# Kernel optimization log

Measured on AMD Instinct MI355X. Metric: run time of the kernel, lower is better.

Reference implementation:

```python
import jax, jax.numpy as jnp
import numpy as np
import math

B, S, D, H, E = 4, 4096, 256, 8, 262144
HD = D // H
ITER_NUM = 4
TEMP = 1.0
LN_EPS = 1e-12
N = B * S


def setup_inputs() -> dict:
    key = jax.random.key(0)
    ks = jax.random.split(key, 6)
    return {
        "hidden_states": jax.random.normal(ks[0], (B, S, D), dtype=jnp.float32),
        "attention_mask": jnp.zeros((B, S), dtype=jnp.float32),
        "src": jax.random.randint(ks[1], (E,), 0, N),
        "dst": jax.random.randint(ks[2], (E,), 0, N),
        "Wqkv": jax.random.normal(ks[3], (D, 3 * D), dtype=jnp.float32) * 0.02,
        "bqkv": jnp.zeros((3 * D,), dtype=jnp.float32),
        "Wo": jax.random.normal(ks[4], (D, D), dtype=jnp.float32) * 0.02,
        "bo": jnp.zeros((D,), dtype=jnp.float32),
        "gamma": jnp.ones((D,), dtype=jnp.float32),
        "beta": jnp.zeros((D,), dtype=jnp.float32),
    }


def _gn_attn(hidden_states, attention_mask, src, dst, Wqkv, bqkv, Wo, bo, gamma, beta):
    # qkv projection (node ordering is batch-major: node = b*S + s)
    qkv = hidden_states @ Wqkv + bqkv                      # [B,S,3D]
    q, k, v = jnp.split(qkv, 3, axis=-1)
    q = q / math.sqrt(HD)
    qn = q.reshape(N, H, HD)
    kn = k.reshape(N, H, HD)
    vn = v.reshape(N, H, HD)
    node_mask = (attention_mask >= 0).reshape(N)           # [N] bool

    # per-edge dot-product scores: u_dot_v('k','q') -> dot(k[src], q[dst])
    score = jnp.einsum("ehd,ehd->eh", kn[src], qn[dst])    # [E,H]
    edge_mask = node_mask[src] & node_mask[dst]
    score = jnp.where(edge_mask[:, None], score, jnp.float32(-10000.0))

    # edge softmax over incoming edges of each dst node (per head)
    mx = jax.ops.segment_max(score, dst, num_segments=N)   # [N,H]
    es = jnp.exp(score - mx[dst])
    den = jax.ops.segment_sum(es, dst, num_segments=N)     # [N,H]
    attn = es / den[dst]                                   # [E,H]

    # diffusion (heat-kernel / PPR-style) message passing
    h = math.exp(-TEMP) * vn                               # [N,H,HD]
    gather = h
    fact = 1.0
    for ki in range(1, ITER_NUM):
        msg = attn[:, :, None] * h[src]                    # [E,H,HD]
        h = jax.ops.segment_sum(msg, dst, num_segments=N)  # [N,H,HD]
        fact = fact * (TEMP / ki)
        gather = gather + fact * h

    attn_out = gather.reshape(B, S, D)

    # output projection + residual + LayerNorm
    y = attn_out @ Wo + bo + hidden_states
    mu = jnp.mean(y, axis=-1, keepdims=True)
    var = jnp.mean(jnp.square(y - mu), axis=-1, keepdims=True)
    return (y - mu) / jnp.sqrt(var + LN_EPS) * gamma + beta


def reference(hidden_states, attention_mask, src, dst, Wqkv, bqkv, Wo, bo, gamma, beta):
    return _gn_attn(hidden_states, attention_mask, src, dst, Wqkv, bqkv, Wo, bo, gamma, beta)
```

## Files before the change

kernel.cpp:

```cpp
#include <hip/hip_runtime.h>
#include <math.h>

#define NN 16384
#define DD 256
#define HH 8
#define EE 262144
#define D3 768
#define QSCALE 0.17677669529663687f
#define EXPN1 0.36787944117144233f
#define LN_EPS 1e-12f

typedef short bf16x8 __attribute__((ext_vector_type(8)));
typedef float f32x4 __attribute__((ext_vector_type(4)));
typedef float f32x2 __attribute__((ext_vector_type(2)));
typedef unsigned short u16;
typedef unsigned char u8;

__device__ __forceinline__ float bf_lo(unsigned u) { return __uint_as_float(u << 16); }
__device__ __forceinline__ float bf_hi(unsigned u) { return __uint_as_float(u & 0xffff0000u); }
__device__ __forceinline__ unsigned f2bf(float f) {
    unsigned b = __float_as_uint(f);
    return (b + 0x7fffu + ((b >> 16) & 1u)) >> 16;
}
__device__ __forceinline__ unsigned pack2bf(float lo, float hi) {
    return f2bf(lo) | (f2bf(hi) << 16);
}
__device__ __forceinline__ u8 f2fp8(float v) {
    return (u8)(__builtin_amdgcn_cvt_pk_fp8_f32(v, v, 0, false) & 0xff);
}

__global__ void prep_kernel(const float* __restrict__ hidden, unsigned* __restrict__ hidb,
                            const float* __restrict__ Wqkv, const float* __restrict__ bqkv,
                            u16* __restrict__ WtQ, float* __restrict__ biasq,
                            const float* __restrict__ Wo, const float* __restrict__ bo,
                            u16* __restrict__ WtO, float* __restrict__ biaso,
                            const int* __restrict__ dst, int* __restrict__ deg) {
    int b = blockIdx.x;
    if (b < 4096) {
        int gid = b * 256 + threadIdx.x;
        float4 v = *(const float4*)(hidden + (size_t)gid * 4);
        *(uint2*)(hidb + (size_t)gid * 2) = make_uint2(pack2bf(v.x, v.y), pack2bf(v.z, v.w));
    } else if (b < 4864) {
        int gid = (b - 4096) * 256 + threadIdx.x;
        int n = gid >> 8, k = gid & 255;
        float s = (n < DD) ? QSCALE : 1.0f;
        WtQ[(size_t)n * 256 + k] = (u16)f2bf(Wqkv[(size_t)k * D3 + n] * s);
        if (k == 0) biasq[n] = bqkv[n] * s;
    } else if (b < 5120) {
        int gid = (b - 4864) * 256 + threadIdx.x;
        int n = gid >> 8, k = gid & 255;
        WtO[(size_t)n * 256 + k] = (u16)f2bf(Wo[(size_t)k * DD + n]);
        if (k == 0) biaso[n] = bo[n];
    } else {
        int e = (b - 5120) * 256 + threadIdx.x;
        atomicAdd(&deg[dst[e]], 1);
    }
}

__global__ __launch_bounds__(256) void mfma_gemm1_kernel(
        const u16* __restrict__ Ab, const u16* __restrict__ Bt,
        const float* __restrict__ bias,
        u16* __restrict__ qb, u8* __restrict__ kb8,
        u8* __restrict__ h8, u16* __restrict__ gb) {
    __shared__ u16 As[128 * 40];
    __shared__ u16 Bs[128 * 40];
    const int tid = threadIdx.x;
    const int m0 = blockIdx.y * 128;
    const int n0 = blockIdx.x * 128;
    const int wave = tid >> 6, lane = tid & 63;
    const int wr = wave >> 1, wc = wave & 1;
    const int lm = lane & 15, quad = lane >> 4;

    f32x4 acc[4][4] = {};
    const int r0 = tid >> 2;
    const int c8 = (tid & 3) * 8;

    for (int k0 = 0; k0 < 256; k0 += 32) {
        #pragma unroll
        for (int s = 0; s < 2; ++s) {
            int r = r0 + s * 64;
            *(uint4*)&As[r * 40 + c8] = *(const uint4*)(Ab + (size_t)(m0 + r) * 256 + k0 + c8);
            *(uint4*)&Bs[r * 40 + c8] = *(const uint4*)(Bt + (size_t)(n0 + r) * 256 + k0 + c8);
        }
        __syncthreads();
        bf16x8 af[4], bfv[4];
        #pragma unroll
        for (int mi = 0; mi < 4; ++mi)
            af[mi] = *(const bf16x8*)&As[(wr * 64 + mi * 16 + lm) * 40 + quad * 8];
        #pragma unroll
        for (int ni = 0; ni < 4; ++ni)
            bfv[ni] = *(const bf16x8*)&Bs[(wc * 64 + ni * 16 + lm) * 40 + quad * 8];
        #pragma unroll
        for (int mi = 0; mi < 4; ++mi)
            #pragma unroll
            for (int ni = 0; ni < 4; ++ni)
                acc[mi][ni] = __builtin_amdgcn_mfma_f32_16x16x32_bf16(
                    af[mi], bfv[ni], acc[mi][ni], 0, 0, 0);
        __syncthreads();
    }

    const int type = n0 >> 8;
    const int cb = n0 & 255;
    #pragma unroll
    for (int mi = 0; mi < 4; ++mi) {
        #pragma unroll
        for (int j = 0; j < 4; ++j) {
            int m = m0 + wr * 64 + mi * 16 + quad * 4 + j;
            #pragma unroll
            for (int ni = 0; ni < 4; ++ni) {
                int nl = wc * 64 + ni * 16 + lm;
                float val = acc[mi][ni][j] + bias[n0 + nl];
                size_t off = (size_t)m * 256 + cb + nl;
                if (type == 0) qb[off] = (u16)f2bf(val);
                else if (type == 1) kb8[off] = f2fp8(val);
                else {
                    float hx = val * EXPN1;
                    h8[off] = f2fp8(hx);
                    gb[off] = (u16)f2bf(hx);
                }
            }
        }
    }
}

__global__ __launch_bounds__(1024) void scan_kernel(const int* __restrict__ deg,
                                                    int* __restrict__ offs,
                                                    int* __restrict__ cursor, int n) {
    __shared__ int part[1024];
    int t = threadIdx.x;
    int base = t * 16;
    int local[16];
    int s = 0;
    #pragma unroll
    for (int i = 0; i < 16; ++i) { local[i] = s; s += deg[base + i]; }
    part[t] = s;
    __syncthreads();
    for (int d = 1; d < 1024; d <<= 1) {
        int add = (t >= d) ? part[t - d] : 0;
        __syncthreads();
        part[t] += add;
        __syncthreads();
    }
    int excl = part[t] - s;
    #pragma unroll
    for (int i = 0; i < 16; ++i) {
        offs[base + i] = excl + local[i];
        cursor[base + i] = excl + local[i];
    }
    if (t == 1023) offs[n] = excl + s;
}

__global__ void scatter_kernel(const int* __restrict__ src, const int* __restrict__ dst,
                               int* __restrict__ cursor, int* __restrict__ srcs) {
    int e = blockIdx.x * 256 + threadIdx.x;
    int pos = atomicAdd(&cursor[dst[e]], 1);
    srcs[pos] = src[e];
}

__global__ __launch_bounds__(256) void edge_softmax_kernel(
        const unsigned* __restrict__ qb, const u8* __restrict__ kb8,
        const int* __restrict__ offs, const int* __restrict__ srcs,
        const float* __restrict__ amask, float* __restrict__ attn,
        float* __restrict__ inv) {
    const int wave = threadIdx.x >> 6, lane = threadIdx.x & 63;
    const int node = blockIdx.x * 4 + wave;
    const int h = lane & 7;
    const int eo = lane >> 3;
    const int beg = offs[node], end = offs[node + 1];
    const uint4* qp = (const uint4*)(qb + (size_t)node * 128 + h * 16);
    uint4 q0 = qp[0], q1 = qp[1], q2 = qp[2], q3 = qp[3];
    unsigned qq[16] = {q0.x, q0.y, q0.z, q0.w, q1.x, q1.y, q1.z, q1.w,
                       q2.x, q2.y, q2.z, q2.w, q3.x, q3.y, q3.z, q3.w};
    const bool dvalid = amask[node] >= 0.0f;

    float m = -1e30f;
    for (int i0 = beg; i0 < end; i0 += 8) {
        int i = i0 + eo;
        if (i < end) {
            int s = srcs[i];
            const uint4* kp = (const uint4*)(kb8 + (size_t)s * 256 + h * 32);
            uint4 k0 = kp[0], k1 = kp[1];
            unsigned kk[8] = {k0.x, k0.y, k0.z, k0.w, k1.x, k1.y, k1.z, k1.w};
            float acc = 0.0f;
            #pragma unroll
            for (int t = 0; t < 8; ++t) {
                f32x2 a = __builtin_amdgcn_cvt_pk_f32_fp8(kk[t], false);
                f32x2 b = __builtin_amdgcn_cvt_pk_f32_fp8(kk[t], true);
                acc += a.x * bf_lo(qq[2 * t]) + a.y * bf_hi(qq[2 * t]);
                acc += b.x * bf_lo(qq[2 * t + 1]) + b.y * bf_hi(qq[2 * t + 1]);
            }
            bool valid = dvalid && (amask[s] >= 0.0f);
            float score = valid ? acc : -10000.0f;
            attn[(size_t)i * 8 + h] = score;
            m = fmaxf(m, score);
        }
    }
    m = fmaxf(m, __shfl_xor(m, 8));
    m = fmaxf(m, __shfl_xor(m, 16));
    m = fmaxf(m, __shfl_xor(m, 32));

    float den = 0.0f;
    for (int i0 = beg; i0 < end; i0 += 8) {
        int i = i0 + eo;
        if (i < end) {
            float es = __expf(attn[(size_t)i * 8 + h] - m);
            attn[(size_t)i * 8 + h] = es;
            den += es;
        }
    }
    den += __shfl_xor(den, 8);
    den += __shfl_xor(den, 16);
    den += __shfl_xor(den, 32);
    if (lane < 8) inv[node * 8 + h] = (end > beg) ? 1.0f / den : 0.0f;
}

__global__ void diffuse_kernel(const int* __restrict__ offs, const int* __restrict__ srcs,
                               const float* __restrict__ attn, const float* __restrict__ inv,
                               const unsigned* __restrict__ hcur, unsigned* __restrict__ hnext,
                               uint2* __restrict__ gb, float fact) {
    int gid = blockIdx.x * 256 + threadIdx.x;
    int node = gid >> 6;
    int j2 = gid & 63;
    int h = j2 >> 3;
    int beg = offs[node], end = offs[node + 1];
    float a0 = 0.0f, a1 = 0.0f, a2 = 0.0f, a3 = 0.0f;
    int i = beg;
    for (; i + 8 <= end; i += 8) {
        int sarr[8]; float aarr[8]; unsigned hv[8];
        #pragma unroll
        for (int t = 0; t < 8; ++t) {
            sarr[t] = srcs[i + t];
            aarr[t] = attn[(size_t)(i + t) * 8 + h];
        }
        #pragma unroll
        for (int t = 0; t < 8; ++t) hv[t] = hcur[(size_t)sarr[t] * 64 + j2];
        #pragma unroll
        for (int t = 0; t < 8; ++t) {
            float a = aarr[t];
            f32x2 lo = __builtin_amdgcn_cvt_pk_f32_fp8(hv[t], false);
            f32x2 hi = __builtin_amdgcn_cvt_pk_f32_fp8(hv[t], true);
            a0 += a * lo.x; a1 += a * lo.y;
            a2 += a * hi.x; a3 += a * hi.y;
        }
    }
    if (i < end) {
        int cnt = end - i;
        int sarr[8]; float aarr[8]; unsigned hv[8];
        #pragma unroll
        for (int t = 0; t < 8; ++t) if (t < cnt) {
            sarr[t] = srcs[i + t];
            aarr[t] = attn[(size_t)(i + t) * 8 + h];
        }
        #pragma unroll
        for (int t = 0; t < 8; ++t) if (t < cnt) hv[t] = hcur[(size_t)sarr[t] * 64 + j2];
        #pragma unroll
        for (int t = 0; t < 8; ++t) if (t < cnt) {
            float a = aarr[t];
            f32x2 lo = __builtin_amdgcn_cvt_pk_f32_fp8(hv[t], false);
            f32x2 hi = __builtin_amdgcn_cvt_pk_f32_fp8(hv[t], true);
            a0 += a * lo.x; a1 += a * lo.y;
            a2 += a * hi.x; a3 += a * hi.y;
        }
    }
    float iv = inv[node * 8 + h];
    a0 *= iv; a1 *= iv; a2 *= iv; a3 *= iv;
    if (hnext) {
        int pk = __builtin_amdgcn_cvt_pk_fp8_f32(a0, a1, 0, false);
        pk = __builtin_amdgcn_cvt_pk_fp8_f32(a2, a3, pk, true);
        hnext[(size_t)node * 64 + j2] = (unsigned)pk;
    }
    uint2* gp = gb + (size_t)node * 64 + j2;
    uint2 g = *gp;
    float g0 = bf_lo(g.x) + fact * a0;
    float g1 = bf_hi(g.x) + fact * a1;
    float g2 = bf_lo(g.y) + fact * a2;
    float g3 = bf_hi(g.y) + fact * a3;
    *gp = make_uint2(pack2bf(g0, g1), pack2bf(g2, g3));
}

__global__ __launch_bounds__(256) void gemm2_ln_kernel(
        const u16* __restrict__ Ab, const u16* __restrict__ Bt,
        const float* __restrict__ bias, const float* __restrict__ resid,
        const float* __restrict__ gamma, const float* __restrict__ beta,
        float* __restrict__ out) {
    __shared__ u16 As[64 * 40];
    __shared__ u16 Bs[256 * 40];
    const int tid = threadIdx.x;
    const int m0 = blockIdx.x * 64;
    const int wave = tid >> 6, lane = tid & 63;
    const int lm = lane & 15, quad = lane >> 4;

    f32x4 acc[16] = {};
    for (int k0 = 0; k0 < 256; k0 += 32) {
        *(uint4*)&As[(tid >> 2) * 40 + (tid & 3) * 8] =
            *(const uint4*)(Ab + (size_t)(m0 + (tid >> 2)) * 256 + k0 + (tid & 3) * 8);
        {
            const uint4* srcp = (const uint4*)(Bt + (size_t)tid * 256 + k0);
            uint4* dstp = (uint4*)&Bs[tid * 40];
            dstp[0] = srcp[0]; dstp[1] = srcp[1]; dstp[2] = srcp[2]; dstp[3] = srcp[3];
        }
        __syncthreads();
        bf16x8 af = *(const bf16x8*)&As[(wave * 16 + lm) * 40 + quad * 8];
        #pragma unroll
        for (int ni = 0; ni < 16; ++ni) {
            bf16x8 bfv = *(const bf16x8*)&Bs[(ni * 16 + lm) * 40 + quad * 8];
            acc[ni] = __builtin_amdgcn_mfma_f32_16x16x32_bf16(af, bfv, acc[ni], 0, 0, 0);
        }
        __syncthreads();
    }

    const int mrow = m0 + wave * 16 + quad * 4;
    float ga[16], be[16];
    float rowsum[4] = {}, rowsq[4] = {};
    #pragma unroll
    for (int ni = 0; ni < 16; ++ni) {
        int col = ni * 16 + lm;
        float bia = bias[col];
        ga[ni] = gamma[col]; be[ni] = beta[col];
        #pragma unroll
        for (int j = 0; j < 4; ++j) {
            float val = acc[ni][j] + bia + resid[(size_t)(mrow + j) * 256 + col];
            acc[ni][j] = val;
            rowsum[j] += val;
            rowsq[j] += val * val;
        }
    }
    #pragma unroll
    for (int j = 0; j < 4; ++j) {
        #pragma unroll
        for (int msk = 1; msk <= 8; msk <<= 1) {
            rowsum[j] += __shfl_xor(rowsum[j], msk);
            rowsq[j] += __shfl_xor(rowsq[j], msk);
        }
    }
    float mu[4], rstd[4];
    #pragma unroll
    for (int j = 0; j < 4; ++j) {
        mu[j] = rowsum[j] * (1.0f / 256.0f);
        float var = rowsq[j] * (1.0f / 256.0f) - mu[j] * mu[j];
        rstd[j] = 1.0f / sqrtf(var + LN_EPS);
    }
    #pragma unroll
    for (int ni = 0; ni < 16; ++ni) {
        int col = ni * 16 + lm;
        #pragma unroll
        for (int j = 0; j < 4; ++j)
            out[(size_t)(mrow + j) * 256 + col] = (acc[ni][j] - mu[j]) * rstd[j] * ga[ni] + be[ni];
    }
}

extern "C" void kernel_launch(void* const* d_in, const int* in_sizes, int n_in,
                              void* d_out, int out_size, void* d_ws, size_t ws_size,
                              hipStream_t stream) {
    const float* hidden = (const float*)d_in[0];
    const float* amask  = (const float*)d_in[1];
    const int*   src    = (const int*)d_in[2];
    const int*   dst    = (const int*)d_in[3];
    const float* Wqkv   = (const float*)d_in[4];
    const float* bqkv   = (const float*)d_in[5];
    const float* Wo     = (const float*)d_in[6];
    const float* bo     = (const float*)d_in[7];
    const float* gamma  = (const float*)d_in[8];
    const float* beta   = (const float*)d_in[9];
    float* out = (float*)d_out;

    char* p = (char*)d_ws;
    u16*      hidb   = (u16*)p;      p += (size_t)NN * DD * 2;
    u16*      WtQ    = (u16*)p;      p += (size_t)D3 * DD * 2;
    u16*      WtO    = (u16*)p;      p += (size_t)DD * DD * 2;
    float*    biasq  = (float*)p;    p += (size_t)D3 * 4;
    float*    biaso  = (float*)p;    p += (size_t)DD * 4;
    u16*      qb     = (u16*)p;      p += (size_t)NN * DD * 2;
    u8*       kb8    = (u8*)p;       p += (size_t)NN * DD;
    u8*       h8A    = (u8*)p;       p += (size_t)NN * DD;
    u8*       h8B    = (u8*)p;       p += (size_t)NN * DD;
    u16*      gb     = (u16*)p;      p += (size_t)NN * DD * 2;
    float*    attn   = (float*)p;    p += (size_t)EE * HH * 4;
    float*    inv    = (float*)p;    p += (size_t)NN * HH * 4;
    int*      deg    = (int*)p;      p += (size_t)NN * 4;
    int*      offs   = (int*)p;      p += (size_t)(NN + 1) * 4;
    int*      cursor = (int*)p;      p += (size_t)NN * 4;
    int*      srcs   = (int*)p;      p += (size_t)EE * 4;

    hipMemsetAsync(deg, 0, (size_t)NN * 4, stream);
    prep_kernel<<<6144, 256, 0, stream>>>(hidden, (unsigned*)hidb,
                                          Wqkv, bqkv, WtQ, biasq,
                                          Wo, bo, WtO, biaso, dst, deg);

    scan_kernel<<<1, 1024, 0, stream>>>(deg, offs, cursor, NN);
    scatter_kernel<<<EE / 256, 256, 0, stream>>>(src, dst, cursor, srcs);

    mfma_gemm1_kernel<<<dim3(D3 / 128, NN / 128), 256, 0, stream>>>(
        hidb, WtQ, biasq, qb, kb8, h8A, gb);

    edge_softmax_kernel<<<NN / 4, 256, 0, stream>>>(
        (const unsigned*)qb, kb8, offs, srcs, amask, attn, inv);

    diffuse_kernel<<<(NN * 64) / 256, 256, 0, stream>>>(
        offs, srcs, attn, inv, (const unsigned*)h8A, (unsigned*)h8B, (uint2*)gb, 1.0f);
    diffuse_kernel<<<(NN * 64) / 256, 256, 0, stream>>>(
        offs, srcs, attn, inv, (const unsigned*)h8B, (unsigned*)h8A, (uint2*)gb, 0.5f);
    diffuse_kernel<<<(NN * 64) / 256, 256, 0, stream>>>(
        offs, srcs, attn, inv, (const unsigned*)h8A, nullptr, (uint2*)gb, 1.0f / 6.0f);

    gemm2_ln_kernel<<<NN / 64, 256, 0, stream>>>(
        gb, WtO, biaso, hidden, gamma, beta, out);
}
```

Measured before the change: 224.8 us.

## Fuse edge softmax and three diffusion steps into one cooperative persistent kernel

Replaces the edge-softmax kernel and the three diffusion launches with a single cooperative kernel of 1024 blocks that separates phases with grid.sync(). Each wave handles four nodes. For low-degree nodes the scores stay in registers and the normalised attention is written once, which removes the separate inv array and the re-reads of attn. The running gather sum is kept in registers across steps rather than read and written to gb on every step. The cost is grid-wide barriers and an occupancy requirement of 4 blocks per CU, and it relies on a cooperative launch succeeding.

```diff
diff --git a/kernel.cpp b/kernel.cpp
--- a/kernel.cpp
+++ b/kernel.cpp
@@ -1,5 +1,8 @@
 #include <hip/hip_runtime.h>
+#include <hip/hip_cooperative_groups.h>
 #include <math.h>
+
+namespace cg = cooperative_groups;
 
 #define NN 16384
 #define DD 256
@@ -157,72 +160,28 @@
     srcs[pos] = src[e];
 }
 
-__global__ __launch_bounds__(256) void edge_softmax_kernel(
-        const unsigned* __restrict__ qb, const u8* __restrict__ kb8,
-        const int* __restrict__ offs, const int* __restrict__ srcs,
-        const float* __restrict__ amask, float* __restrict__ attn,
-        float* __restrict__ inv) {
-    const int wave = threadIdx.x >> 6, lane = threadIdx.x & 63;
-    const int node = blockIdx.x * 4 + wave;
-    const int h = lane & 7;
-    const int eo = lane >> 3;
-    const int beg = offs[node], end = offs[node + 1];
-    const uint4* qp = (const uint4*)(qb + (size_t)node * 128 + h * 16);
-    uint4 q0 = qp[0], q1 = qp[1], q2 = qp[2], q3 = qp[3];
-    unsigned qq[16] = {q0.x, q0.y, q0.z, q0.w, q1.x, q1.y, q1.z, q1.w,
-                       q2.x, q2.y, q2.z, q2.w, q3.x, q3.y, q3.z, q3.w};
-    const bool dvalid = amask[node] >= 0.0f;
-
-    float m = -1e30f;
-    for (int i0 = beg; i0 < end; i0 += 8) {
-        int i = i0 + eo;
-        if (i < end) {
-            int s = srcs[i];
-            const uint4* kp = (const uint4*)(kb8 + (size_t)s * 256 + h * 32);
-            uint4 k0 = kp[0], k1 = kp[1];
-            unsigned kk[8] = {k0.x, k0.y, k0.z, k0.w, k1.x, k1.y, k1.z, k1.w};
-            float acc = 0.0f;
-            #pragma unroll
-            for (int t = 0; t < 8; ++t) {
-                f32x2 a = __builtin_amdgcn_cvt_pk_f32_fp8(kk[t], false);
-                f32x2 b = __builtin_amdgcn_cvt_pk_f32_fp8(kk[t], true);
-                acc += a.x * bf_lo(qq[2 * t]) + a.y * bf_hi(qq[2 * t]);
-                acc += b.x * bf_lo(qq[2 * t + 1]) + b.y * bf_hi(qq[2 * t + 1]);
-            }
-            bool valid = dvalid && (amask[s] >= 0.0f);
-            float score = valid ? acc : -10000.0f;
-            attn[(size_t)i * 8 + h] = score;
-            m = fmaxf(m, score);
-        }
-    }
-    m = fmaxf(m, __shfl_xor(m, 8));
-    m = fmaxf(m, __shfl_xor(m, 16));
-    m = fmaxf(m, __shfl_xor(m, 32));
-
-    float den = 0.0f;
-    for (int i0 = beg; i0 < end; i0 += 8) {
-        int i = i0 + eo;
-        if (i < end) {
-            float es = __expf(attn[(size_t)i * 8 + h] - m);
-            attn[(size_t)i * 8 + h] = es;
-            den += es;
-        }
-    }
-    den += __shfl_xor(den, 8);
-    den += __shfl_xor(den, 16);
-    den += __shfl_xor(den, 32);
-    if (lane < 8) inv[node * 8 + h] = (end > beg) ? 1.0f / den : 0.0f;
-}
-
-__global__ void diffuse_kernel(const int* __restrict__ offs, const int* __restrict__ srcs,
-                               const float* __restrict__ attn, const float* __restrict__ inv,
-                               const unsigned* __restrict__ hcur, unsigned* __restrict__ hnext,
-                               uint2* __restrict__ gb, float fact) {
-    int gid = blockIdx.x * 256 + threadIdx.x;
-    int node = gid >> 6;
-    int j2 = gid & 63;
-    int h = j2 >> 3;
-    int beg = offs[node], end = offs[node + 1];
+
+__device__ __forceinline__ float edge_score(const unsigned qq[16], const u8* __restrict__ kb8,
+                                            const float* __restrict__ amask,
+                                            int s, int h, bool dvalid) {
+    const uint4* kp = (const uint4*)(kb8 + (size_t)s * 256 + h * 32);
+    uint4 k0 = kp[0], k1 = kp[1];
+    unsigned kk[8] = {k0.x, k0.y, k0.z, k0.w, k1.x, k1.y, k1.z, k1.w};
+    float acc = 0.0f;
+    #pragma unroll
+    for (int t = 0; t < 8; ++t) {
+        f32x2 a = __builtin_amdgcn_cvt_pk_f32_fp8(kk[t], false);
+        f32x2 b = __builtin_amdgcn_cvt_pk_f32_fp8(kk[t], true);
+        acc += a.x * bf_lo(qq[2 * t]) + a.y * bf_hi(qq[2 * t]);
+        acc += b.x * bf_lo(qq[2 * t + 1]) + b.y * bf_hi(qq[2 * t + 1]);
+    }
+    bool valid = dvalid && (amask[s] >= 0.0f);
+    return valid ? acc : -10000.0f;
+}
+
+__device__ __forceinline__ float4 gather_node(int beg, int end, int h, int j2,
+        const int* __restrict__ srcs, const float* __restrict__ attn,
+        const unsigned* __restrict__ hcur) {
     float a0 = 0.0f, a1 = 0.0f, a2 = 0.0f, a3 = 0.0f;
     int i = beg;
     for (; i + 8 <= end; i += 8) {
@@ -262,20 +221,139 @@
             a2 += a * hi.x; a3 += a * hi.y;
         }
     }
-    float iv = inv[node * 8 + h];
-    a0 *= iv; a1 *= iv; a2 *= iv; a3 *= iv;
-    if (hnext) {
-        int pk = __builtin_amdgcn_cvt_pk_fp8_f32(a0, a1, 0, false);
-        pk = __builtin_amdgcn_cvt_pk_fp8_f32(a2, a3, pk, true);
-        hnext[(size_t)node * 64 + j2] = (unsigned)pk;
-    }
-    uint2* gp = gb + (size_t)node * 64 + j2;
-    uint2 g = *gp;
-    float g0 = bf_lo(g.x) + fact * a0;
-    float g1 = bf_hi(g.x) + fact * a1;
-    float g2 = bf_lo(g.y) + fact * a2;
-    float g3 = bf_hi(g.y) + fact * a3;
-    *gp = make_uint2(pack2bf(g0, g1), pack2bf(g2, g3));
+    return make_float4(a0, a1, a2, a3);
+}
+
+__global__ __launch_bounds__(256, 4) void fused_graph_kernel(
+        const unsigned* __restrict__ qb, const u8* __restrict__ kb8,
+        const int* __restrict__ offs, const int* __restrict__ srcs,
+        const float* __restrict__ amask, float* __restrict__ attn,
+        unsigned* __restrict__ hA, unsigned* __restrict__ hB,
+        uint2* __restrict__ gb) {
+    cg::grid_group grid = cg::this_grid();
+    const int wave = threadIdx.x >> 6, lane = threadIdx.x & 63;
+    const int gwave = blockIdx.x * 4 + wave;
+
+    {
+        const int h = lane & 7;
+        const int eo = lane >> 3;
+        #pragma unroll 1
+        for (int k = 0; k < 4; ++k) {
+            const int node = gwave + k * 4096;
+            const int beg = offs[node], end = offs[node + 1];
+            const int cnt = end - beg;
+            const uint4* qp = (const uint4*)(qb + (size_t)node * 128 + h * 16);
+            uint4 q0 = qp[0], q1 = qp[1], q2 = qp[2], q3 = qp[3];
+            unsigned qq[16] = {q0.x, q0.y, q0.z, q0.w, q1.x, q1.y, q1.z, q1.w,
+                               q2.x, q2.y, q2.z, q2.w, q3.x, q3.y, q3.z, q3.w};
+            const bool dvalid = amask[node] >= 0.0f;
+            float m = -1e30f;
+            if (cnt <= 64) {
+                float esb[8];
+                #pragma unroll
+                for (int it = 0; it < 8; ++it) {
+                    int i = beg + it * 8 + eo;
+                    float sc = -1e30f;
+                    if (i < end) sc = edge_score(qq, kb8, amask, srcs[i], h, dvalid);
+                    esb[it] = sc;
+                    m = fmaxf(m, sc);
+                }
+                m = fmaxf(m, __shfl_xor(m, 8));
+                m = fmaxf(m, __shfl_xor(m, 16));
+                m = fmaxf(m, __shfl_xor(m, 32));
+                float den = 0.0f;
+                #pragma unroll
+                for (int it = 0; it < 8; ++it) {
+                    int i = beg + it * 8 + eo;
+                    if (i < end) { float es = __expf(esb[it] - m); esb[it] = es; den += es; }
+                }
+                den += __shfl_xor(den, 8);
+                den += __shfl_xor(den, 16);
+                den += __shfl_xor(den, 32);
+                float iv = (cnt > 0) ? 1.0f / den : 0.0f;
+                #pragma unroll
+                for (int it = 0; it < 8; ++it) {
+                    int i = beg + it * 8 + eo;
+                    if (i < end) attn[(size_t)i * 8 + h] = esb[it] * iv;
+                }
+            } else {
+                for (int i0 = beg; i0 < end; i0 += 8) {
+                    int i = i0 + eo;
+                    if (i < end) {
+                        float sc = edge_score(qq, kb8, amask, srcs[i], h, dvalid);
+                        attn[(size_t)i * 8 + h] = sc;
+                        m = fmaxf(m, sc);
+                    }
+                }
+                m = fmaxf(m, __shfl_xor(m, 8));
+                m = fmaxf(m, __shfl_xor(m, 16));
+                m = fmaxf(m, __shfl_xor(m, 32));
+                float den = 0.0f;
+                for (int i0 = beg; i0 < end; i0 += 8) {
+                    int i = i0 + eo;
+                    if (i < end) {
+                        float es = __expf(attn[(size_t)i * 8 + h] - m);
+                        attn[(size_t)i * 8 + h] = es;
+                        den += es;
+                    }
+                }
+                den += __shfl_xor(den, 8);
+                den += __shfl_xor(den, 16);
+                den += __shfl_xor(den, 32);
+                float iv = 1.0f / den;
+                for (int i0 = beg; i0 < end; i0 += 8) {
+                    int i = i0 + eo;
+                    if (i < end) attn[(size_t)i * 8 + h] *= iv;
+                }
+            }
+        }
+    }
+    grid.sync();
+
+    const int j2 = lane;
+    const int hh = lane >> 3;
+    float4 accg[4];
+
+    #pragma unroll
+    for (int k = 0; k < 4; ++k) {
+        const int node = gwave + k * 4096;
+        float4 a = gather_node(offs[node], offs[node + 1], hh, j2, srcs, attn, hA);
+        uint2 g = gb[(size_t)node * 64 + j2];
+        accg[k].x = bf_lo(g.x) + a.x;
+        accg[k].y = bf_hi(g.x) + a.y;
+        accg[k].z = bf_lo(g.y) + a.z;
+        accg[k].w = bf_hi(g.y) + a.w;
+        int pk = __builtin_amdgcn_cvt_pk_fp8_f32(a.x, a.y, 0, false);
+        pk = __builtin_amdgcn_cvt_pk_fp8_f32(a.z, a.w, pk, true);
+        hB[(size_t)node * 64 + j2] = (unsigned)pk;
+    }
+    grid.sync();
+
+    #pragma unroll
+    for (int k = 0; k < 4; ++k) {
+        const int node = gwave + k * 4096;
+        float4 a = gather_node(offs[node], offs[node + 1], hh, j2, srcs, attn, hB);
+        accg[k].x += 0.5f * a.x;
+        accg[k].y += 0.5f * a.y;
+        accg[k].z += 0.5f * a.z;
+        accg[k].w += 0.5f * a.w;
+        int pk = __builtin_amdgcn_cvt_pk_fp8_f32(a.x, a.y, 0, false);
+        pk = __builtin_amdgcn_cvt_pk_fp8_f32(a.z, a.w, pk, true);
+        hA[(size_t)node * 64 + j2] = (unsigned)pk;
+    }
+    grid.sync();
+
+    const float f3 = 1.0f / 6.0f;
+    #pragma unroll
+    for (int k = 0; k < 4; ++k) {
+        const int node = gwave + k * 4096;
+        float4 a = gather_node(offs[node], offs[node + 1], hh, j2, srcs, attn, hA);
+        float g0 = accg[k].x + f3 * a.x;
+        float g1 = accg[k].y + f3 * a.y;
+        float g2 = accg[k].z + f3 * a.z;
+        float g3 = accg[k].w + f3 * a.w;
+        gb[(size_t)node * 64 + j2] = make_uint2(pack2bf(g0, g1), pack2bf(g2, g3));
+    }
 }
 
 __global__ __launch_bounds__(256) void gemm2_ln_kernel(
@@ -376,7 +454,6 @@
     u8*       h8B    = (u8*)p;       p += (size_t)NN * DD;
     u16*      gb     = (u16*)p;      p += (size_t)NN * DD * 2;
     float*    attn   = (float*)p;    p += (size_t)EE * HH * 4;
-    float*    inv    = (float*)p;    p += (size_t)NN * HH * 4;
     int*      deg    = (int*)p;      p += (size_t)NN * 4;
     int*      offs   = (int*)p;      p += (size_t)(NN + 1) * 4;
     int*      cursor = (int*)p;      p += (size_t)NN * 4;
@@ -393,15 +470,22 @@
     mfma_gemm1_kernel<<<dim3(D3 / 128, NN / 128), 256, 0, stream>>>(
         hidb, WtQ, biasq, qb, kb8, h8A, gb);
 
-    edge_softmax_kernel<<<NN / 4, 256, 0, stream>>>(
-        (const unsigned*)qb, kb8, offs, srcs, amask, attn, inv);
-
-    diffuse_kernel<<<(NN * 64) / 256, 256, 0, stream>>>(
-        offs, srcs, attn, inv, (const unsigned*)h8A, (unsigned*)h8B, (uint2*)gb, 1.0f);
-    diffuse_kernel<<<(NN * 64) / 256, 256, 0, stream>>>(
-        offs, srcs, attn, inv, (const unsigned*)h8B, (unsigned*)h8A, (uint2*)gb, 0.5f);
-    diffuse_kernel<<<(NN * 64) / 256, 256, 0, stream>>>(
-        offs, srcs, attn, inv, (const unsigned*)h8A, nullptr, (uint2*)gb, 1.0f / 6.0f);
+    {
+        const unsigned* qbu = (const unsigned*)qb;
+        const u8* kb8c = kb8;
+        const int* offsc = offs;
+        const int* srcsc = srcs;
+        const float* amaskc = amask;
+        float* attnp = attn;
+        unsigned* hAu = (unsigned*)h8A;
+        unsigned* hBu = (unsigned*)h8B;
+        uint2* gbu = (uint2*)gb;
+        void* args[] = {(void*)&qbu, (void*)&kb8c, (void*)&offsc, (void*)&srcsc,
+                        (void*)&amaskc, (void*)&attnp, (void*)&hAu, (void*)&hBu,
+                        (void*)&gbu};
+        hipLaunchCooperativeKernel((const void*)fused_graph_kernel,
+                                   dim3(1024), dim3(256), args, 0, stream);
+    }
 
     gemm2_ln_kernel<<<NN / 64, 256, 0, stream>>>(
         gb, WtO, biaso, hidden, gamma, beta, out);
```

Result: slower. 607.2 us (+170.2%).
